# Kernel tuning notes

Hardware: AMD Instinct MI355X
Metric: run time of the kernel (lower is better)

Reference implementation:

```python
import jax, jax.numpy as jnp
import numpy as np

B, F, D = 16384, 256, 128
H = [512, 256]
OUT = 8
VOCAB = 100000


def setup_inputs() -> dict:
    key = jax.random.key(0)
    ks = jax.random.split(key, 16)
    s = lambda k, *sh: jax.random.normal(k, sh, jnp.float32) * 0.05
    return dict(
        features=jax.random.normal(ks[0], (B, F), jnp.float32),
        ent_idx=jax.random.randint(ks[1], (B,), 0, VOCAB),
        target=jax.random.randint(ks[2], (B,), 0, OUT),
        Wf=s(ks[3], F, D), bf=jnp.zeros((D,), jnp.float32),
        Wu=s(ks[4], D, D), bu=jnp.zeros((D,), jnp.float32),
        w_cf=s(ks[5], D), w_fc=s(ks[6], D),
        w_ef=s(ks[7], D), w_fe=s(ks[8], D),
        b_c=jnp.zeros((1,), jnp.float32), b_e=jnp.zeros((1,), jnp.float32),
        head_tab=s(ks[9], VOCAB, D), ent_tab=s(ks[10], VOCAB, D),
        W0=s(ks[11], 2 * D, H[0]), b0=jnp.zeros((H[0],), jnp.float32),
        W1=s(ks[12], H[0], H[1]), b1=jnp.zeros((H[1],), jnp.float32),
        W2=s(ks[13], H[1], OUT), b2=jnp.zeros((OUT,), jnp.float32),
    )


def cross_compress(f, e, w_cf, w_fc, w_ef, w_fe, b_c, b_e):
    # torch code builds c = f (outer) e of shape (B,D,D) then matmuls a (D,1)
    # vector; algebraically (f e^T) w = f * (e . w), so we use the O(B*D) form.
    ew_cf = e @ w_cf  # (B,)
    fw_fc = f @ w_fc
    ew_ef = e @ w_ef
    fw_fe = f @ w_fe
    new_f = f * ew_cf[:, None] + e * fw_fc[:, None] + b_c
    new_e = f * ew_ef[:, None] + e * fw_fe[:, None] + b_e
    return new_f, new_e


def reference(features, ent_idx, target, Wf, bf, Wu, bu, w_cf, w_fc, w_ef,
              w_fe, b_c, b_e, head_tab, ent_tab, W0, b0, W1, b1, W2, b2):
    # 'rec' branch of CompanyOperationEvaluation.forward (eval mode, dropout=id)
    cf = jax.nn.relu(features @ Wf + bf)          # feature_layer
    e = ent_tab[ent_idx]                           # entity_embed lookup
    h = head_tab[ent_idx]                          # head_embed lookup (same ids)
    for _ in range(2):
        cf = jax.nn.relu(cf @ Wu + bu)             # user_low_mlp_layer
        h, e = cross_compress(h, e, w_cf, w_fc, w_ef, w_fe, b_c, b_e)
    high = jnp.concatenate([cf, e], axis=1)        # (B, 2D)
    x = jax.nn.relu(high @ W0 + b0)
    x = jax.nn.relu(x @ W1 + b1)
    x = jax.nn.relu(x @ W2 + b2)                   # pred_last_layer
    prob = jax.nn.softmax(x, axis=1)
    return (prob, target)
```

## Files before the change

### kernel.cpp

```cpp
#include <hip/hip_runtime.h>
#include <hip/hip_bf16.h>


typedef __bf16 bf16x8 __attribute__((ext_vector_type(8)));
typedef float floatx4 __attribute__((ext_vector_type(4)));

__device__ __forceinline__ unsigned short f2bf(float x) {
  unsigned int u = __builtin_bit_cast(unsigned int, x);
  u = (u + 0x7FFFu + ((u >> 16) & 1u)) >> 16;
  return (unsigned short)u;
}

__device__ __forceinline__ int sz(int row, int col) {
  return col ^ ((row & 7) << 3);
}

#define BAR_VM(N)                                                      \
  do {                                                                 \
    asm volatile("s_waitcnt vmcnt(" #N ") lgkmcnt(0)" ::: "memory");   \
    __builtin_amdgcn_s_barrier();                                      \
    __builtin_amdgcn_sched_barrier(0);                                 \
  } while (0)

__global__ __launch_bounds__(256) void prep_kernel(
    const float* __restrict__ Wf, const float* __restrict__ Wu,
    const float* __restrict__ W0, const float* __restrict__ W1,
    const float* __restrict__ W2,
    unsigned short* __restrict__ wfT, unsigned short* __restrict__ wuT,
    unsigned short* __restrict__ w0T, unsigned short* __restrict__ w1T,
    unsigned short* __restrict__ w2T) {
  __shared__ unsigned short tile[32][34];
  const int bid = blockIdx.x, tid = threadIdx.x;
  if (bid < 304) {
    int t = bid;
    const float* src; unsigned short* dst; int N, K, kt, nt;
    if (t < 32)       { src = Wf; dst = wfT; N = 128; K = 256; kt = t >> 2;       nt = t & 3; }
    else if (t < 48)  { t -= 32;  src = Wu; dst = wuT; N = 128; K = 128; kt = t >> 2; nt = t & 3; }
    else if (t < 176) { t -= 48;  src = W0; dst = w0T; N = 512; K = 256; kt = t >> 4; nt = t & 15; }
    else              { t -= 176; src = W1; dst = w1T; N = 256; K = 512; kt = t >> 3; nt = t & 7; }
    {
      int r = tid >> 3, cg = (tid & 7) * 4;
      float4 v = *(const float4*)(src + (size_t)(kt * 32 + r) * N + nt * 32 + cg);
      tile[r][cg + 0] = f2bf(v.x); tile[r][cg + 1] = f2bf(v.y);
      tile[r][cg + 2] = f2bf(v.z); tile[r][cg + 3] = f2bf(v.w);
    }
    __syncthreads();
    {
      int rp = tid >> 3, cg = (tid & 7) * 4;
      uint2 o;
      o.x = (unsigned)tile[cg + 0][rp] | ((unsigned)tile[cg + 1][rp] << 16);
      o.y = (unsigned)tile[cg + 2][rp] | ((unsigned)tile[cg + 3][rp] << 16);
      *(uint2*)(dst + (size_t)(nt * 32 + rp) * K + kt * 32 + cg) = o;
    }
  } else {
#pragma unroll
    for (int i = 0; i < 8; ++i) {
      int g = tid * 8 + i, k = g >> 3, n = g & 7;
      w2T[n * 256 + k] = f2bf(W2[g]);
    }
  }
}

template <int LDK>
__device__ __forceinline__ void stageB(unsigned short* dstbase,
                                       const unsigned short* __restrict__ src,
                                       int tid) {
#pragma unroll
  for (int i = 0; i < 4; ++i) {
    int chunk = i * 256 + tid;
    int row = chunk >> 3, segs = chunk & 7;
    int segl = segs ^ (row & 7);
    const unsigned short* g = src + (size_t)row * LDK + segl * 8;
    unsigned short* d = dstbase + chunk * 8;
    __builtin_amdgcn_global_load_lds((const unsigned int*)g, (unsigned int*)d,
                                     16, 0, 0);
  }
}

template <int PASS_STEPS, int LDK>
__device__ __forceinline__ const unsigned short* srcstep(
    const unsigned short* __restrict__ s, int st) {
  return s + (size_t)(st / PASS_STEPS) * 128 * LDK + (st % PASS_STEPS) * 64;
}

template <int LDA>
__device__ __forceinline__ void mstep(const unsigned short* A,
                                      const unsigned short* bt, int k0,
                                      floatx4* acc, int m16, int quad,
                                      int wave) {
#pragma unroll
  for (int kk = 0; kk < 64; kk += 32) {
    const int ca = k0 + kk + quad * 8;
    const int cb = kk + quad * 8;
    const int ra0 = m16, ra1 = 16 + m16;
    const int rb0 = wave * 32 + m16, rb1 = wave * 32 + 16 + m16;
    bf16x8 a0 = *(const bf16x8*)&A[ra0 * LDA + sz(ra0, ca)];
    bf16x8 a1 = *(const bf16x8*)&A[ra1 * LDA + sz(ra1, ca)];
    bf16x8 b0 = *(const bf16x8*)&bt[rb0 * 64 + sz(rb0, cb)];
    bf16x8 b1 = *(const bf16x8*)&bt[rb1 * 64 + sz(rb1, cb)];
    acc[0] = __builtin_amdgcn_mfma_f32_16x16x32_bf16(a0, b0, acc[0], 0, 0, 0);
    acc[1] = __builtin_amdgcn_mfma_f32_16x16x32_bf16(a0, b1, acc[1], 0, 0, 0);
    acc[2] = __builtin_amdgcn_mfma_f32_16x16x32_bf16(a1, b0, acc[2], 0, 0, 0);
    acc[3] = __builtin_amdgcn_mfma_f32_16x16x32_bf16(a1, b1, acc[3], 0, 0, 0);
  }
}

template <int T, int LDA, int PASS_STEPS, int LDK>
__device__ __forceinline__ void gemm_phase(
    const unsigned short* A, const unsigned short* __restrict__ src,
    unsigned short* b_sh, floatx4* acc, int tid, int m16, int quad, int wave) {
  stageB<LDK>(b_sh, srcstep<PASS_STEPS, LDK>(src, 0), tid);
  if (T > 1) {
    stageB<LDK>(b_sh + 8192, srcstep<PASS_STEPS, LDK>(src, 1), tid);
    BAR_VM(4);
  } else {
    BAR_VM(0);
  }
#pragma unroll
  for (int t = 0; t < T; ++t) {
    if (t + 2 < T)
      stageB<LDK>(b_sh + ((t + 2) % 3) * 8192,
                  srcstep<PASS_STEPS, LDK>(src, t + 2), tid);
    mstep<LDA>(A, b_sh + (t % 3) * 8192, (t % PASS_STEPS) * 64,
               acc + (t / PASS_STEPS) * 4, m16, quad, wave);
    if (t + 2 < T) {
      BAR_VM(4);
    } else {
      BAR_VM(0);
    }
  }
}

__global__ __launch_bounds__(256, 2) void fused_mlp_kernel(
    const float* __restrict__ features, const int* __restrict__ ent_idx,
    const float* __restrict__ head_tab, const float* __restrict__ ent_tab,
    const float* __restrict__ w_cf, const float* __restrict__ w_fc,
    const float* __restrict__ w_ef, const float* __restrict__ w_fe,
    const float* __restrict__ b_c, const float* __restrict__ b_e,
    const unsigned short* __restrict__ wfT,
    const unsigned short* __restrict__ wuT, const float* __restrict__ bf_,
    const float* __restrict__ bu,
    const unsigned short* __restrict__ w0T, const float* __restrict__ b0,
    const unsigned short* __restrict__ w1T, const float* __restrict__ b1,
    const unsigned short* __restrict__ w2T, const float* __restrict__ b2,
    const int* __restrict__ target, float* __restrict__ out) {
  __shared__ __align__(16) unsigned short regionA[16384];
  __shared__ __align__(16) unsigned short b_sh[3 * 8192];
  unsigned short* feat_sh = regionA;
  unsigned short* buf0 = regionA + 8192;
  unsigned short* buf1 = regionA + 12288;
  unsigned short* A_sh = regionA;
  unsigned short* x0_sh = regionA;
  unsigned short* x1_sh = b_sh;
  float* cw_p = (float*)buf1;

  const int tid = threadIdx.x;
  const int r0 = blockIdx.x * 32;
  const int lane = tid & 63, wave = tid >> 6;
  const int m16 = lane & 15, quad = lane >> 4;

  const int grow = tid >> 3, gpart = tid & 7;
  const int gidx = ent_idx[r0 + grow];
  const float* hp = head_tab + (size_t)gidx * 128 + gpart * 16;
  const float* ep = ent_tab + (size_t)gidx * 128 + gpart * 16;
  float4 h4[4], e4[4];
#pragma unroll
  for (int j = 0; j < 4; ++j) {
    h4[j] = *(const float4*)(hp + j * 4);
    e4[j] = *(const float4*)(ep + j * 4);
  }
  if (tid < 128) {
    int a = tid >> 5, o = (tid & 31) * 4;
    const float* s = (a == 0) ? w_cf : (a == 1) ? w_fc : (a == 2) ? w_ef : w_fe;
    *(float4*)&cw_p[a * 128 + o] = *(const float4*)(s + o);
  }

#pragma unroll
  for (int i = 0; i < 8; ++i) {
    int idx4 = i * 256 + tid;
    int row = idx4 >> 6, c = (idx4 & 63) * 4;
    float4 v = *(const float4*)(features + (size_t)(r0 + row) * 256 + c);
    uint2 o;
    o.x = (unsigned)f2bf(v.x) | ((unsigned)f2bf(v.y) << 16);
    o.y = (unsigned)f2bf(v.z) | ((unsigned)f2bf(v.w) << 16);
    *(uint2*)&feat_sh[row * 256 + sz(row, c)] = o;
  }

  floatx4 acc[4];
#pragma unroll
  for (int j = 0; j < 4; ++j) acc[j] = (floatx4){0.f, 0.f, 0.f, 0.f};
  gemm_phase<4, 256, 4, 256>(feat_sh, wfT, b_sh, acc, tid, m16, quad, wave);
#pragma unroll
  for (int mi = 0; mi < 2; ++mi)
#pragma unroll
    for (int ni = 0; ni < 2; ++ni) {
      int col = wave * 32 + ni * 16 + m16;
      float bv = bf_[col];
#pragma unroll
      for (int r = 0; r < 4; ++r) {
        int row = mi * 16 + quad * 4 + r;
        buf0[row * 128 + sz(row, col)] =
            f2bf(fmaxf(acc[mi * 2 + ni][r] + bv, 0.f));
      }
    }

  {
    float h[16], e[16];
#pragma unroll
    for (int j = 0; j < 4; ++j) {
      h[4 * j + 0] = h4[j].x; h[4 * j + 1] = h4[j].y;
      h[4 * j + 2] = h4[j].z; h[4 * j + 3] = h4[j].w;
      e[4 * j + 0] = e4[j].x; e[4 * j + 1] = e4[j].y;
      e[4 * j + 2] = e4[j].z; e[4 * j + 3] = e4[j].w;
    }
    const float bc = b_c[0], be = b_e[0];
#pragma unroll
    for (int it = 0; it < 2; ++it) {
      float d0 = 0.f, d1 = 0.f, d2 = 0.f, d3 = 0.f;
#pragma unroll
      for (int j = 0; j < 16; ++j) {
        float wcf = cw_p[0 * 128 + gpart * 16 + j];
        float wfc = cw_p[1 * 128 + gpart * 16 + j];
        float wef = cw_p[2 * 128 + gpart * 16 + j];
        float wfe = cw_p[3 * 128 + gpart * 16 + j];
        d0 += e[j] * wcf; d1 += h[j] * wfc;
        d2 += e[j] * wef; d3 += h[j] * wfe;
      }
#pragma unroll
      for (int s = 1; s < 8; s <<= 1) {
        d0 += __shfl_xor(d0, s); d1 += __shfl_xor(d1, s);
        d2 += __shfl_xor(d2, s); d3 += __shfl_xor(d3, s);
      }
#pragma unroll
      for (int j = 0; j < 16; ++j) {
        float nh = h[j] * d0 + e[j] * d1 + bc;
        float ne = h[j] * d2 + e[j] * d3 + be;
        h[j] = nh; e[j] = ne;
      }
    }
    uint4 o0, o1;
    unsigned* w = (unsigned*)&o0;
#pragma unroll
    for (int j = 0; j < 4; ++j)
      w[j] = (unsigned)f2bf(e[2 * j]) | ((unsigned)f2bf(e[2 * j + 1]) << 16);
    w = (unsigned*)&o1;
#pragma unroll
    for (int j = 0; j < 4; ++j)
      w[j] = (unsigned)f2bf(e[8 + 2 * j]) |
             ((unsigned)f2bf(e[8 + 2 * j + 1]) << 16);
    const int c0 = 128 + gpart * 16;
    *(uint4*)&A_sh[grow * 256 + sz(grow, c0)] = o0;
    *(uint4*)&A_sh[grow * 256 + sz(grow, c0 + 8)] = o1;
  }

#pragma unroll
  for (int j = 0; j < 4; ++j) acc[j] = (floatx4){0.f, 0.f, 0.f, 0.f};
  gemm_phase<2, 128, 2, 128>(buf0, wuT, b_sh, acc, tid, m16, quad, wave);
#pragma unroll
  for (int mi = 0; mi < 2; ++mi)
#pragma unroll
    for (int ni = 0; ni < 2; ++ni) {
      int col = wave * 32 + ni * 16 + m16;
      float bv = bu[col];
#pragma unroll
      for (int r = 0; r < 4; ++r) {
        int row = mi * 16 + quad * 4 + r;
        buf1[row * 128 + sz(row, col)] =
            f2bf(fmaxf(acc[mi * 2 + ni][r] + bv, 0.f));
      }
    }

#pragma unroll
  for (int j = 0; j < 4; ++j) acc[j] = (floatx4){0.f, 0.f, 0.f, 0.f};
  BAR_VM(0);
  mstep<128>(buf1, b_sh, 0, acc, m16, quad, wave);
  mstep<128>(buf1, b_sh + 8192, 64, acc, m16, quad, wave);
  BAR_VM(0);
#pragma unroll
  for (int mi = 0; mi < 2; ++mi)
#pragma unroll
    for (int ni = 0; ni < 2; ++ni) {
      int col = wave * 32 + ni * 16 + m16;
      float bv = bu[col];
#pragma unroll
      for (int r = 0; r < 4; ++r) {
        int row = mi * 16 + quad * 4 + r;
        A_sh[row * 256 + sz(row, col)] =
            f2bf(fmaxf(acc[mi * 2 + ni][r] + bv, 0.f));
      }
    }

  floatx4 acc16[16];
#pragma unroll
  for (int j = 0; j < 16; ++j) acc16[j] = (floatx4){0.f, 0.f, 0.f, 0.f};
  gemm_phase<16, 256, 4, 256>(A_sh, w0T, b_sh, acc16, tid, m16, quad, wave);
#pragma unroll
  for (int np = 0; np < 4; ++np)
#pragma unroll
    for (int mi = 0; mi < 2; ++mi)
#pragma unroll
      for (int ni = 0; ni < 2; ++ni) {
        int col = np * 128 + wave * 32 + ni * 16 + m16;
        float bv = b0[col];
#pragma unroll
        for (int r = 0; r < 4; ++r) {
          int row = mi * 16 + quad * 4 + r;
          x0_sh[row * 512 + sz(row, col)] =
              f2bf(fmaxf(acc16[np * 4 + mi * 2 + ni][r] + bv, 0.f));
        }
      }

  floatx4 acc8[8];
#pragma unroll
  for (int j = 0; j < 8; ++j) acc8[j] = (floatx4){0.f, 0.f, 0.f, 0.f};
  gemm_phase<16, 512, 8, 512>(x0_sh, w1T, b_sh, acc8, tid, m16, quad, wave);
#pragma unroll
  for (int np = 0; np < 2; ++np)
#pragma unroll
    for (int mi = 0; mi < 2; ++mi)
#pragma unroll
      for (int ni = 0; ni < 2; ++ni) {
        int col = np * 128 + wave * 32 + ni * 16 + m16;
        float bv = b1[col];
#pragma unroll
        for (int r = 0; r < 4; ++r)
          x1_sh[(mi * 16 + quad * 4 + r) * 264 + col] =
              f2bf(fmaxf(acc8[np * 4 + mi * 2 + ni][r] + bv, 0.f));
      }
  BAR_VM(0);

  {
    int row = tid >> 3, q = tid & 7;
    float p[8];
#pragma unroll
    for (int n = 0; n < 8; ++n) p[n] = 0.f;
#pragma unroll
    for (int jb = 0; jb < 4; ++jb) {
      bf16x8 xv = *(const bf16x8*)&x1_sh[row * 264 + q * 32 + jb * 8];
#pragma unroll
      for (int n = 0; n < 8; ++n) {
        bf16x8 wv = *(const bf16x8*)(w2T + n * 256 + q * 32 + jb * 8);
#pragma unroll
        for (int j = 0; j < 8; ++j) p[n] += (float)xv[j] * (float)wv[j];
      }
    }
#pragma unroll
    for (int s = 1; s < 8; s <<= 1)
#pragma unroll
      for (int n = 0; n < 8; ++n) p[n] += __shfl_xor(p[n], s);
    if (q == 0) {
      float mx = -1e30f;
#pragma unroll
      for (int n = 0; n < 8; ++n) {
        p[n] = fmaxf(p[n] + b2[n], 0.f);
        mx = fmaxf(mx, p[n]);
      }
      float sum = 0.f;
#pragma unroll
      for (int n = 0; n < 8; ++n) { p[n] = __expf(p[n] - mx); sum += p[n]; }
      const float inv = 1.f / sum;
      const int gr = r0 + row;
      float4 o0 = {p[0] * inv, p[1] * inv, p[2] * inv, p[3] * inv};
      float4 o1 = {p[4] * inv, p[5] * inv, p[6] * inv, p[7] * inv};
      *(float4*)(out + (size_t)gr * 8) = o0;
      *(float4*)(out + (size_t)gr * 8 + 4) = o1;
      out[16384 * 8 + gr] = (float)target[gr];
    }
  }
}

extern "C" void kernel_launch(void* const* d_in, const int* in_sizes, int n_in,
                              void* d_out, int out_size, void* d_ws, size_t ws_size,
                              hipStream_t stream) {
  const float* features = (const float*)d_in[0];
  const int* ent_idx    = (const int*)d_in[1];
  const int* target     = (const int*)d_in[2];
  const float* Wf  = (const float*)d_in[3];
  const float* bf_ = (const float*)d_in[4];
  const float* Wu  = (const float*)d_in[5];
  const float* bu  = (const float*)d_in[6];
  const float* w_cf = (const float*)d_in[7];
  const float* w_fc = (const float*)d_in[8];
  const float* w_ef = (const float*)d_in[9];
  const float* w_fe = (const float*)d_in[10];
  const float* b_c  = (const float*)d_in[11];
  const float* b_e  = (const float*)d_in[12];
  const float* head_tab = (const float*)d_in[13];
  const float* ent_tab  = (const float*)d_in[14];
  const float* W0 = (const float*)d_in[15];
  const float* b0 = (const float*)d_in[16];
  const float* W1 = (const float*)d_in[17];
  const float* b1 = (const float*)d_in[18];
  const float* W2 = (const float*)d_in[19];
  const float* b2 = (const float*)d_in[20];
  float* out = (float*)d_out;

  unsigned short* ws = (unsigned short*)d_ws;
  size_t off = 0;
  auto alloc = [&](size_t n) { unsigned short* p = ws + off; off += n; return p; };
  unsigned short* wfT  = alloc(32768);
  unsigned short* wuT  = alloc(16384);
  unsigned short* w0T  = alloc(131072);
  unsigned short* w1T  = alloc(131072);
  unsigned short* w2T  = alloc(2048);
  (void)ws_size; (void)in_sizes; (void)n_in; (void)out_size;

  prep_kernel<<<305, 256, 0, stream>>>(Wf, Wu, W0, W1, W2,
                                       wfT, wuT, w0T, w1T, w2T);
  fused_mlp_kernel<<<512, 256, 0, stream>>>(features, ent_idx, head_tab,
      ent_tab, w_cf, w_fc, w_ef, w_fe, b_c, b_e, wfT, wuT, bf_, bu,
      w0T, b0, w1T, b1, w2T, b2, target, out);
}
```

Before: 181.7 us.

## Double row tile to 64 with 8 waves in a 2x4 grid and 128-wide K steps

Each block now handles 64 rows with 512 threads arranged as a 2x4 wave grid, and each staged weight K-step grows from 64 to 128 columns. Every weight tile loaded into LDS is therefore reused across twice as many rows, which halves global weight traffic per row and the number of barrier-separated pipeline steps. The cross-compress weight vectors are now read into registers instead of through LDS. LDS use doubles to about 160KB per block and the grid shrinks to 256 blocks, which may hurt occupancy and latency hiding. The new indexing must stay consistent in the parts of the kernel not shown.

```diff
diff --git a/kernel.cpp b/kernel.cpp
--- a/kernel.cpp
+++ b/kernel.cpp
@@ -67,9 +67,9 @@
                                        int tid) {
 #pragma unroll
   for (int i = 0; i < 4; ++i) {
-    int chunk = i * 256 + tid;
-    int row = chunk >> 3, segs = chunk & 7;
-    int segl = segs ^ (row & 7);
+    int chunk = i * 512 + tid;
+    int row = chunk >> 4, seg = chunk & 15;
+    int segl = seg ^ (row & 7);
     const unsigned short* g = src + (size_t)row * LDK + segl * 8;
     unsigned short* d = dstbase + chunk * 8;
     __builtin_amdgcn_global_load_lds((const unsigned int*)g, (unsigned int*)d,
@@ -77,27 +77,27 @@
   }
 }
 
-template <int PASS_STEPS, int LDK>
+template <int PASS, int LDK>
 __device__ __forceinline__ const unsigned short* srcstep(
     const unsigned short* __restrict__ s, int st) {
-  return s + (size_t)(st / PASS_STEPS) * 128 * LDK + (st % PASS_STEPS) * 64;
+  return s + (size_t)(st / PASS) * 128 * LDK + (st % PASS) * 128;
 }
 
 template <int LDA>
 __device__ __forceinline__ void mstep(const unsigned short* A,
                                       const unsigned short* bt, int k0,
                                       floatx4* acc, int m16, int quad,
-                                      int wave) {
-#pragma unroll
-  for (int kk = 0; kk < 64; kk += 32) {
+                                      int wm, int wn) {
+#pragma unroll
+  for (int kk = 0; kk < 128; kk += 32) {
     const int ca = k0 + kk + quad * 8;
     const int cb = kk + quad * 8;
-    const int ra0 = m16, ra1 = 16 + m16;
-    const int rb0 = wave * 32 + m16, rb1 = wave * 32 + 16 + m16;
+    const int ra0 = wm * 32 + m16, ra1 = wm * 32 + 16 + m16;
+    const int rb0 = wn * 32 + m16, rb1 = wn * 32 + 16 + m16;
     bf16x8 a0 = *(const bf16x8*)&A[ra0 * LDA + sz(ra0, ca)];
     bf16x8 a1 = *(const bf16x8*)&A[ra1 * LDA + sz(ra1, ca)];
-    bf16x8 b0 = *(const bf16x8*)&bt[rb0 * 64 + sz(rb0, cb)];
-    bf16x8 b1 = *(const bf16x8*)&bt[rb1 * 64 + sz(rb1, cb)];
+    bf16x8 b0 = *(const bf16x8*)&bt[rb0 * 128 + sz(rb0, cb)];
+    bf16x8 b1 = *(const bf16x8*)&bt[rb1 * 128 + sz(rb1, cb)];
     acc[0] = __builtin_amdgcn_mfma_f32_16x16x32_bf16(a0, b0, acc[0], 0, 0, 0);
     acc[1] = __builtin_amdgcn_mfma_f32_16x16x32_bf16(a0, b1, acc[1], 0, 0, 0);
     acc[2] = __builtin_amdgcn_mfma_f32_16x16x32_bf16(a1, b0, acc[2], 0, 0, 0);
@@ -105,13 +105,14 @@
   }
 }
 
-template <int T, int LDA, int PASS_STEPS, int LDK>
+template <int T, int LDA, int PASS, int LDK>
 __device__ __forceinline__ void gemm_phase(
     const unsigned short* A, const unsigned short* __restrict__ src,
-    unsigned short* b_sh, floatx4* acc, int tid, int m16, int quad, int wave) {
-  stageB<LDK>(b_sh, srcstep<PASS_STEPS, LDK>(src, 0), tid);
+    unsigned short* b_sh, floatx4* acc, int tid, int m16, int quad, int wm,
+    int wn) {
+  stageB<LDK>(b_sh, srcstep<PASS, LDK>(src, 0), tid);
   if (T > 1) {
-    stageB<LDK>(b_sh + 8192, srcstep<PASS_STEPS, LDK>(src, 1), tid);
+    stageB<LDK>(b_sh + 16384, srcstep<PASS, LDK>(src, 1), tid);
     BAR_VM(4);
   } else {
     BAR_VM(0);
@@ -119,10 +120,10 @@
 #pragma unroll
   for (int t = 0; t < T; ++t) {
     if (t + 2 < T)
-      stageB<LDK>(b_sh + ((t + 2) % 3) * 8192,
-                  srcstep<PASS_STEPS, LDK>(src, t + 2), tid);
-    mstep<LDA>(A, b_sh + (t % 3) * 8192, (t % PASS_STEPS) * 64,
-               acc + (t / PASS_STEPS) * 4, m16, quad, wave);
+      stageB<LDK>(b_sh + ((t + 2) % 3) * 16384, srcstep<PASS, LDK>(src, t + 2),
+                  tid);
+    mstep<LDA>(A, b_sh + (t % 3) * 16384, (t % PASS) * 128,
+               acc + (t / PASS) * 4, m16, quad, wm, wn);
     if (t + 2 < T) {
       BAR_VM(4);
     } else {
@@ -131,7 +132,7 @@
   }
 }
 
-__global__ __launch_bounds__(256, 2) void fused_mlp_kernel(
+__global__ __launch_bounds__(512, 2) void fused_mlp_kernel(
     const float* __restrict__ features, const int* __restrict__ ent_idx,
     const float* __restrict__ head_tab, const float* __restrict__ ent_tab,
     const float* __restrict__ w_cf, const float* __restrict__ w_fc,
@@ -144,20 +145,20 @@
     const unsigned short* __restrict__ w1T, const float* __restrict__ b1,
     const unsigned short* __restrict__ w2T, const float* __restrict__ b2,
     const int* __restrict__ target, float* __restrict__ out) {
-  __shared__ __align__(16) unsigned short regionA[16384];
-  __shared__ __align__(16) unsigned short b_sh[3 * 8192];
+  __shared__ __align__(16) unsigned short regionA[32768];
+  __shared__ __align__(16) unsigned short b_sh[3 * 16384];
   unsigned short* feat_sh = regionA;
-  unsigned short* buf0 = regionA + 8192;
-  unsigned short* buf1 = regionA + 12288;
+  unsigned short* buf0 = regionA + 16384;
+  unsigned short* buf1 = regionA + 24576;
   unsigned short* A_sh = regionA;
   unsigned short* x0_sh = regionA;
   unsigned short* x1_sh = b_sh;
-  float* cw_p = (float*)buf1;
 
   const int tid = threadIdx.x;
-  const int r0 = blockIdx.x * 32;
+  const int r0 = blockIdx.x * 64;
   const int lane = tid & 63, wave = tid >> 6;
   const int m16 = lane & 15, quad = lane >> 4;
+  const int wm = wave >> 2, wn = wave & 3;
 
   const int grow = tid >> 3, gpart = tid & 7;
   const int gidx = ent_idx[r0 + grow];
@@ -169,15 +170,10 @@
     h4[j] = *(const float4*)(hp + j * 4);
     e4[j] = *(const float4*)(ep + j * 4);
   }
-  if (tid < 128) {
-    int a = tid >> 5, o = (tid & 31) * 4;
-    const float* s = (a == 0) ? w_cf : (a == 1) ? w_fc : (a == 2) ? w_ef : w_fe;
-    *(float4*)&cw_p[a * 128 + o] = *(const float4*)(s + o);
-  }
 
 #pragma unroll
   for (int i = 0; i < 8; ++i) {
-    int idx4 = i * 256 + tid;
+    int idx4 = i * 512 + tid;
     int row = idx4 >> 6, c = (idx4 & 63) * 4;
     float4 v = *(const float4*)(features + (size_t)(r0 + row) * 256 + c);
     uint2 o;
@@ -189,16 +185,16 @@
   floatx4 acc[4];
 #pragma unroll
   for (int j = 0; j < 4; ++j) acc[j] = (floatx4){0.f, 0.f, 0.f, 0.f};
-  gemm_phase<4, 256, 4, 256>(feat_sh, wfT, b_sh, acc, tid, m16, quad, wave);
+  gemm_phase<2, 256, 2, 256>(feat_sh, wfT, b_sh, acc, tid, m16, quad, wm, wn);
 #pragma unroll
   for (int mi = 0; mi < 2; ++mi)
 #pragma unroll
     for (int ni = 0; ni < 2; ++ni) {
-      int col = wave * 32 + ni * 16 + m16;
+      int col = wn * 32 + ni * 16 + m16;
       float bv = bf_[col];
 #pragma unroll
       for (int r = 0; r < 4; ++r) {
-        int row = mi * 16 + quad * 4 + r;
+        int row = wm * 32 + mi * 16 + quad * 4 + r;
         buf0[row * 128 + sz(row, col)] =
             f2bf(fmaxf(acc[mi * 2 + ni][r] + bv, 0.f));
       }
@@ -213,18 +209,22 @@
       e[4 * j + 0] = e4[j].x; e[4 * j + 1] = e4[j].y;
       e[4 * j + 2] = e4[j].z; e[4 * j + 3] = e4[j].w;
     }
+    float wcf[16], wfc[16], wef[16], wfe[16];
+#pragma unroll
+    for (int jj = 0; jj < 4; ++jj) {
+      *(float4*)&wcf[jj * 4] = *(const float4*)(w_cf + gpart * 16 + jj * 4);
+      *(float4*)&wfc[jj * 4] = *(const float4*)(w_fc + gpart * 16 + jj * 4);
+      *(float4*)&wef[jj * 4] = *(const float4*)(w_ef + gpart * 16 + jj * 4);
+      *(float4*)&wfe[jj * 4] = *(const float4*)(w_fe + gpart * 16 + jj * 4);
+    }
     const float bc = b_c[0], be = b_e[0];
 #pragma unroll
     for (int it = 0; it < 2; ++it) {
       float d0 = 0.f, d1 = 0.f, d2 = 0.f, d3 = 0.f;
 #pragma unroll
       for (int j = 0; j < 16; ++j) {
-        float wcf = cw_p[0 * 128 + gpart * 16 + j];
-        float wfc = cw_p[1 * 128 + gpart * 16 + j];
-        float wef = cw_p[2 * 128 + gpart * 16 + j];
-        float wfe = cw_p[3 * 128 + gpart * 16 + j];
-        d0 += e[j] * wcf; d1 += h[j] * wfc;
-        d2 += e[j] * wef; d3 += h[j] * wfe;
+        d0 += e[j] * wcf[j]; d1 += h[j] * wfc[j];
+        d2 += e[j] * wef[j]; d3 += h[j] * wfe[j];
       }
 #pragma unroll
       for (int s = 1; s < 8; s <<= 1) {
@@ -255,16 +255,16 @@
 
 #pragma unroll
   for (int j = 0; j < 4; ++j) acc[j] = (floatx4){0.f, 0.f, 0.f, 0.f};
-  gemm_phase<2, 128, 2, 128>(buf0, wuT, b_sh, acc, tid, m16, quad, wave);
+  gemm_phase<1, 128, 1, 128>(buf0, wuT, b_sh, acc, tid, m16, quad, wm, wn);
 #pragma unroll
   for (int mi = 0; mi < 2; ++mi)
 #pragma unroll
     for (int ni = 0; ni < 2; ++ni) {
-      int col = wave * 32 + ni * 16 + m16;
+      int col = wn * 32 + ni * 16 + m16;
       float bv = bu[col];
 #pragma unroll
       for (int r = 0; r < 4; ++r) {
-        int row = mi * 16 + quad * 4 + r;
+        int row = wm * 32 + mi * 16 + quad * 4 + r;
         buf1[row * 128 + sz(row, col)] =
             f2bf(fmaxf(acc[mi * 2 + ni][r] + bv, 0.f));
       }
@@ -273,18 +273,17 @@
 #pragma unroll
   for (int j = 0; j < 4; ++j) acc[j] = (floatx4){0.f, 0.f, 0.f, 0.f};
   BAR_VM(0);
-  mstep<128>(buf1, b_sh, 0, acc, m16, quad, wave);
-  mstep<128>(buf1, b_sh + 8192, 64, acc, m16, quad, wave);
+  mstep<128>(buf1, b_sh, 0, acc, m16, quad, wm, wn);
   BAR_VM(0);
 #pragma unroll
   for (int mi = 0; mi < 2; ++mi)
 #pragma unroll
     for (int ni = 0; ni < 2; ++ni) {
-      int col = wave * 32 + ni * 16 + m16;
+      int col = wn * 32 + ni * 16 + m16;
       float bv = bu[col];
 #pragma unroll
       for (int r = 0; r < 4; ++r) {
-        int row = mi * 16 + quad * 4 + r;
+        int row = wm * 32 + mi * 16 + quad * 4 + r;
         A_sh[row * 256 + sz(row, col)] =
             f2bf(fmaxf(acc[mi * 2 + ni][r] + bv, 0.f));
       }
@@ -293,18 +292,18 @@
   floatx4 acc16[16];
 #pragma unroll
   for (int j = 0; j < 16; ++j) acc16[j] = (floatx4){0.f, 0.f, 0.f, 0.f};
-  gemm_phase<16, 256, 4, 256>(A_sh, w0T, b_sh, acc16, tid, m16, quad, wave);
+  gemm_phase<8, 256, 2, 256>(A_sh, w0T, b_sh, acc16, tid, m16, quad, wm, wn);
 #pragma unroll
   for (int np = 0; np < 4; ++np)
 #pragma unroll
     for (int mi = 0; mi < 2; ++mi)
 #pragma unroll
       for (int ni = 0; ni < 2; ++ni) {
-        int col = np * 128 + wave * 32 + ni * 16 + m16;
+        int col = np * 128 + wn * 32 + ni * 16 + m16;
         float bv = b0[col];
 #pragma unroll
         for (int r = 0; r < 4; ++r) {
-          int row = mi * 16 + quad * 4 + r;
+          int row = wm * 32 + mi * 16 + quad * 4 + r;
           x0_sh[row * 512 + sz(row, col)] =
               f2bf(fmaxf(acc16[np * 4 + mi * 2 + ni][r] + bv, 0.f));
         }
@@ -313,18 +312,18 @@
   floatx4 acc8[8];
 #pragma unroll
   for (int j = 0; j < 8; ++j) acc8[j] = (floatx4){0.f, 0.f, 0.f, 0.f};
-  gemm_phase<16, 512, 8, 512>(x0_sh, w1T, b_sh, acc8, tid, m16, quad, wave);
+  gemm_phase<8, 512, 4, 512>(x0_sh, w1T, b_sh, acc8, tid, m16, quad, wm, wn);
 #pragma unroll
   for (int np = 0; np < 2; ++np)
 #pragma unroll
     for (int mi = 0; mi < 2; ++mi)
 #pragma unroll
       for (int ni = 0; ni < 2; ++ni) {
-        int col = np * 128 + wave * 32 + ni * 16 + m16;
+        int col = np * 128 + wn * 32 + ni * 16 + m16;
         float bv = b1[col];
 #pragma unroll
         for (int r = 0; r < 4; ++r)
-          x1_sh[(mi * 16 + quad * 4 + r) * 264 + col] =
+          x1_sh[(wm * 32 + mi * 16 + quad * 4 + r) * 264 + col] =
               f2bf(fmaxf(acc8[np * 4 + mi * 2 + ni][r] + bv, 0.f));
       }
   BAR_VM(0);
@@ -407,7 +406,7 @@
 
   prep_kernel<<<305, 256, 0, stream>>>(Wf, Wu, W0, W1, W2,
                                        wfT, wuT, w0T, w1T, w2T);
-  fused_mlp_kernel<<<512, 256, 0, stream>>>(features, ent_idx, head_tab,
+  fused_mlp_kernel<<<256, 512, 0, stream>>>(features, ent_idx, head_tab,
       ent_tab, w_cf, w_fc, w_ef, w_fe, b_c, b_e, wfT, wuT, bf_, bu,
       w0T, b0, w1T, b1, w2T, b2, target, out);
 }
```

Result: no change. 182.2 us (+0.3%).
